# Optimization experiments

Measured on AMD Instinct MI355X. Metric: run time of the kernel, lower is better.

Reference implementation:

```python
import jax, jax.numpy as jnp
import numpy as np
import math

B, S, D = 1, 4096, 512
H, KVH, DH = 8, 4, 64
DH2 = DH // 2
M = int(math.isqrt(S))           # product-key grid side, S == M*M
K = 8                            # top_k
ROPE_BASE = 10000.0


def rope_cos_sin(seq_len, dh, base):
    inv_freq = 1.0 / (base ** (jnp.arange(0, dh, 2, dtype=jnp.float32) / dh))
    t = jnp.arange(seq_len, dtype=jnp.float32)
    freqs = jnp.outer(t, inv_freq)                      # (S, dh/2)
    emb = jnp.concatenate([freqs, freqs], axis=-1)      # (S, dh)
    return jnp.cos(emb), jnp.sin(emb)


def apply_rope(x, cos, sin):
    # x: (B, H, S, dh); half-split rotation (llama-style)
    dh2 = x.shape[-1] // 2
    rot = jnp.concatenate([-x[..., dh2:], x[..., :dh2]], axis=-1)
    return x * cos + rot * sin


def setup_inputs() -> dict:
    key = jax.random.key(0)
    ks = jax.random.split(key, 5)
    s = 0.02
    x = jax.random.normal(ks[0], (B, S, D), dtype=jnp.float32)
    Wq = jax.random.normal(ks[1], (H * DH, D), dtype=jnp.float32) * s
    Wk = jax.random.normal(ks[2], (KVH * DH, D), dtype=jnp.float32) * s
    Wv = jax.random.normal(ks[3], (KVH * DH, D), dtype=jnp.float32) * s
    Wo = jax.random.normal(ks[4], (D, H * DH), dtype=jnp.float32) * s
    return {"x": x, "Wq": Wq, "Wk": Wk, "Wv": Wv, "Wo": Wo}


def reference(x, Wq, Wk, Wv, Wo):
    b, s, d = x.shape
    cos, sin = rope_cos_sin(s, DH, ROPE_BASE)
    q = (x @ Wq.T).reshape(b, s, H, DH).transpose(0, 2, 1, 3)      # (B,H,S,DH)
    k = (x @ Wk.T).reshape(b, s, KVH, DH).transpose(0, 2, 1, 3)    # (B,KVH,S,DH)
    v = (x @ Wv.T).reshape(b, s, KVH, DH).transpose(0, 2, 1, 3)
    q = apply_rope(q, cos, sin)
    k = apply_rope(k, cos, sin)
    rep = H // KVH                                                 # GQA repeat_kv
    k = jnp.repeat(k, rep, axis=1)                                 # (B,H,S,DH)
    v = jnp.repeat(v, rep, axis=1)

    # factorized product keys: sum over grid rows / cols
    kg = k.reshape(b, H, M, M, DH)
    k1 = kg[..., :DH2].sum(axis=-2)                                # (B,H,M,DH2)
    k2 = kg[..., DH2:].sum(axis=-3)                                # (B,H,M,DH2)
    q1, q2 = q[..., :DH2], q[..., DH2:]

    def topk_sel(qh, kh):  # qh: (S,DH2), kh: (M,DH2)
        scores = qh @ kh.T                                         # (S,M)
        _, idx = jax.lax.top_k(scores, K)                          # (S,K)
        return kh[idx], idx                                        # (S,K,DH2), (S,K)

    sel2 = jax.vmap(jax.vmap(topk_sel))
    k1v, i1 = sel2(q1, k1)                                         # (B,H,S,K,DH2)
    k2v, i2 = sel2(q2, k2)

    # cross-product candidates: (B,H,S,K,K,DH) -> (B,H,S,K*K,DH)
    c1 = jnp.broadcast_to(k1v[:, :, :, :, None, :], (b, H, s, K, K, DH2))
    c2 = jnp.broadcast_to(k2v[:, :, :, None, :, :], (b, H, s, K, K, DH2))
    cand = jnp.concatenate([c1, c2], axis=-1).reshape(b, H, s, K * K, DH)

    scores_final = jnp.einsum('bhsd,bhscd->bhsc', q, cand)         # (B,H,S,K*K)
    _, sel = jax.lax.top_k(scores_final, K)                        # (B,H,S,K)
    final_k = jnp.take_along_axis(cand, sel[..., None], axis=3)    # (B,H,S,K,DH)

    row = jnp.take_along_axis(i1, sel // K, axis=3)
    col = jnp.take_along_axis(i2, sel % K, axis=3)
    v_idx = row * M + col                                          # (B,H,S,K)
    final_v = jax.vmap(jax.vmap(lambda vb, ib: vb[ib]))(v, v_idx)  # (B,H,S,K,DH)

    attn = jax.nn.softmax(
        jnp.einsum('bhsd,bhskd->bhsk', q, final_k) / math.sqrt(DH), axis=-1)
    o = jnp.einsum('bhsk,bhskd->bhsd', attn, final_v)              # (B,H,S,DH)
    o = o.transpose(0, 2, 1, 3).reshape(b, s, H * DH)
    return o @ Wo.T
```

## Files before the change

kernel.cpp:

```cpp
#include <hip/hip_runtime.h>
#include <math.h>


static constexpr size_t OFF_P1   = 0;
static constexpr size_t OFF_P2   = 4194304;
static constexpr size_t OFF_Q    = 8388608;
static constexpr size_t OFF_K    = 10485760;
static constexpr size_t OFF_V    = 11534336;
static constexpr size_t OFF_COS  = 12582912;
static constexpr size_t OFF_SIN  = 12713984;
static constexpr size_t OFF_K1   = 12845056;
static constexpr size_t OFF_K2   = 12853248;
static constexpr size_t OFF_O    = 12861440;
static constexpr size_t OFF_PACK = 14958592;

#define LDB 132

__device__ __forceinline__ float rdlane_f(float v, int lane) {
  return __int_as_float(__builtin_amdgcn_readlane(__float_as_int(v), lane));
}

__global__ __launch_bounds__(256) void freq_table_kernel(float* __restrict__ cosT,
    float* __restrict__ sinT) {
  int idx = blockIdx.x * 256 + threadIdx.x;
  int s = idx >> 5;
  int dp = idx & 31;
  double e = (double)dp * (1.0 / 32.0);
  float pf = (float)pow(10000.0, e);
  float invf = 1.0f / pf;
  float argf = __fmul_rn((float)s, invf);
  cosT[idx] = (float)cos((double)argf);
  sinT[idx] = (float)sin((double)argf);
}

__global__ __launch_bounds__(256) void gemm128_qkv(const float* __restrict__ A,
    const float* __restrict__ Wq, const float* __restrict__ Wk,
    const float* __restrict__ Wv, float* __restrict__ C1,
    float* __restrict__ C2) {
  __shared__ float As[16 * LDB];
  __shared__ float Bs[16 * LDB];
  const int tid = threadIdx.x;
  const int z = blockIdx.z;
  const int k0 = z ? 384 : 0;
  const int k1 = z ? 512 : 384;
  float* __restrict__ C = z ? C2 : C1;
  const int bm = blockIdx.y, bn = blockIdx.x;
  const int lrow = tid >> 1;
  const int lko = (tid & 1) << 3;
  const int ty = tid >> 4;
  const int tx = tid & 15;
  const float* Bbase = (bn < 4) ? (Wq + ((size_t)bn * 128) * 512)
                     : (bn < 6) ? (Wk + ((size_t)(bn - 4) * 128) * 512)
                                : (Wv + ((size_t)(bn - 6) * 128) * 512);
  const float* Ap = A + (size_t)(bm * 128 + lrow) * 512 + lko;
  const float* Bp = Bbase + (size_t)lrow * 512 + lko;
  float acc[8][8] = {{0.f}};
  float4 a0 = *(const float4*)(Ap + k0);
  float4 a1 = *(const float4*)(Ap + k0 + 4);
  float4 b0 = *(const float4*)(Bp + k0);
  float4 b1 = *(const float4*)(Bp + k0 + 4);
  for (int kt = k0; kt < k1; kt += 16) {
    __syncthreads();
    As[(lko + 0) * LDB + lrow] = a0.x;
    As[(lko + 1) * LDB + lrow] = a0.y;
    As[(lko + 2) * LDB + lrow] = a0.z;
    As[(lko + 3) * LDB + lrow] = a0.w;
    As[(lko + 4) * LDB + lrow] = a1.x;
    As[(lko + 5) * LDB + lrow] = a1.y;
    As[(lko + 6) * LDB + lrow] = a1.z;
    As[(lko + 7) * LDB + lrow] = a1.w;
    Bs[(lko + 0) * LDB + lrow] = b0.x;
    Bs[(lko + 1) * LDB + lrow] = b0.y;
    Bs[(lko + 2) * LDB + lrow] = b0.z;
    Bs[(lko + 3) * LDB + lrow] = b0.w;
    Bs[(lko + 4) * LDB + lrow] = b1.x;
    Bs[(lko + 5) * LDB + lrow] = b1.y;
    Bs[(lko + 6) * LDB + lrow] = b1.z;
    Bs[(lko + 7) * LDB + lrow] = b1.w;
    __syncthreads();
    if (kt + 16 < k1) {
      a0 = *(const float4*)(Ap + kt + 16);
      a1 = *(const float4*)(Ap + kt + 20);
      b0 = *(const float4*)(Bp + kt + 16);
      b1 = *(const float4*)(Bp + kt + 20);
    }
    #pragma unroll
    for (int k = 0; k < 16; ++k) {
      float4 al = *(const float4*)(&As[k * LDB + (ty << 2)]);
      float4 ah = *(const float4*)(&As[k * LDB + 64 + (ty << 2)]);
      float4 bl = *(const float4*)(&Bs[k * LDB + (tx << 2)]);
      float4 bh = *(const float4*)(&Bs[k * LDB + 64 + (tx << 2)]);
      float af[8] = {al.x, al.y, al.z, al.w, ah.x, ah.y, ah.z, ah.w};
      float bf[8] = {bl.x, bl.y, bl.z, bl.w, bh.x, bh.y, bh.z, bh.w};
      #pragma unroll
      for (int i2 = 0; i2 < 8; ++i2)
        #pragma unroll
        for (int j2 = 0; j2 < 8; ++j2)
          acc[i2][j2] = fmaf(af[i2], bf[j2], acc[i2][j2]);
    }
  }
  #pragma unroll
  for (int i2 = 0; i2 < 8; ++i2) {
    int row = bm * 128 + ((i2 < 4) ? (ty << 2) + i2 : 64 + (ty << 2) + i2 - 4);
    float* Cp = C + (size_t)row * 1024 + bn * 128;
    *(float4*)(Cp + (tx << 2))      = make_float4(acc[i2][0], acc[i2][1], acc[i2][2], acc[i2][3]);
    *(float4*)(Cp + 64 + (tx << 2)) = make_float4(acc[i2][4], acc[i2][5], acc[i2][6], acc[i2][7]);
  }
}

__global__ __launch_bounds__(256) void gemm128_panel(const float* __restrict__ A,
    const float* __restrict__ B, float* __restrict__ C1, float* __restrict__ C2,
    int N, int ksplit) {
  __shared__ float As[16 * LDB];
  __shared__ float Bs[16 * LDB];
  const int tid = threadIdx.x;
  const int z = blockIdx.z;
  const int k0 = z ? ksplit : 0;
  const int k1 = z ? 512 : ksplit;
  float* __restrict__ C = z ? C2 : C1;
  const int bm = blockIdx.y, bn = blockIdx.x;
  const int lrow = tid >> 1;
  const int lko = (tid & 1) << 3;
  const int ty = tid >> 4;
  const int tx = tid & 15;
  const float* Ap = A + (size_t)(bm * 128 + lrow) * 512 + lko;
  const float* Bp = B + (size_t)(bn * 128 + lrow) * 512 + lko;
  float acc[8][8] = {{0.f}};
  float4 a0 = *(const float4*)(Ap + k0);
  float4 a1 = *(const float4*)(Ap + k0 + 4);
  float4 b0 = *(const float4*)(Bp + k0);
  float4 b1 = *(const float4*)(Bp + k0 + 4);
  for (int kt = k0; kt < k1; kt += 16) {
    __syncthreads();
    As[(lko + 0) * LDB + lrow] = a0.x;
    As[(lko + 1) * LDB + lrow] = a0.y;
    As[(lko + 2) * LDB + lrow] = a0.z;
    As[(lko + 3) * LDB + lrow] = a0.w;
    As[(lko + 4) * LDB + lrow] = a1.x;
    As[(lko + 5) * LDB + lrow] = a1.y;
    As[(lko + 6) * LDB + lrow] = a1.z;
    As[(lko + 7) * LDB + lrow] = a1.w;
    Bs[(lko + 0) * LDB + lrow] = b0.x;
    Bs[(lko + 1) * LDB + lrow] = b0.y;
    Bs[(lko + 2) * LDB + lrow] = b0.z;
    Bs[(lko + 3) * LDB + lrow] = b0.w;
    Bs[(lko + 4) * LDB + lrow] = b1.x;
    Bs[(lko + 5) * LDB + lrow] = b1.y;
    Bs[(lko + 6) * LDB + lrow] = b1.z;
    Bs[(lko + 7) * LDB + lrow] = b1.w;
    __syncthreads();
    if (kt + 16 < k1) {
      a0 = *(const float4*)(Ap + kt + 16);
      a1 = *(const float4*)(Ap + kt + 20);
      b0 = *(const float4*)(Bp + kt + 16);
      b1 = *(const float4*)(Bp + kt + 20);
    }
    #pragma unroll
    for (int k = 0; k < 16; ++k) {
      float4 al = *(const float4*)(&As[k * LDB + (ty << 2)]);
      float4 ah = *(const float4*)(&As[k * LDB + 64 + (ty << 2)]);
      float4 bl = *(const float4*)(&Bs[k * LDB + (tx << 2)]);
      float4 bh = *(const float4*)(&Bs[k * LDB + 64 + (tx << 2)]);
      float af[8] = {al.x, al.y, al.z, al.w, ah.x, ah.y, ah.z, ah.w};
      float bf[8] = {bl.x, bl.y, bl.z, bl.w, bh.x, bh.y, bh.z, bh.w};
      #pragma unroll
      for (int i2 = 0; i2 < 8; ++i2)
        #pragma unroll
        for (int j2 = 0; j2 < 8; ++j2)
          acc[i2][j2] = fmaf(af[i2], bf[j2], acc[i2][j2]);
    }
  }
  #pragma unroll
  for (int i2 = 0; i2 < 8; ++i2) {
    int row = bm * 128 + ((i2 < 4) ? (ty << 2) + i2 : 64 + (ty << 2) + i2 - 4);
    float* Cp = C + (size_t)row * N + bn * 128;
    *(float4*)(Cp + (tx << 2))      = make_float4(acc[i2][0], acc[i2][1], acc[i2][2], acc[i2][3]);
    *(float4*)(Cp + 64 + (tx << 2)) = make_float4(acc[i2][4], acc[i2][5], acc[i2][6], acc[i2][7]);
  }
}

__global__ __launch_bounds__(256) void combine_kernel(const float* __restrict__ p1,
    const float* __restrict__ p2, float* __restrict__ out) {
  int i = blockIdx.x * 256 + threadIdx.x;
  out[i] = __fadd_rn(p1[i], p2[i]);
}

__global__ __launch_bounds__(256) void rope_reshape_kernel(const float* __restrict__ p1,
    const float* __restrict__ p2, const float* __restrict__ cosT,
    const float* __restrict__ sinT, float* __restrict__ qb,
    float* __restrict__ kb, float* __restrict__ vb) {
  int idx = blockIdx.x * 256 + threadIdx.x;
  int s = idx >> 10;
  int n = idx & 1023;
  float val = __fadd_rn(p1[idx], p2[idx]);
  int d = n & 63;
  if (n < 768) {
    int dp = d & 31;
    float cs = cosT[(s << 5) + dp];
    float sn = sinT[(s << 5) + dp];
    int npart = (n - d) + ((d < 32) ? d + 32 : d - 32);
    int pidx = (s << 10) + npart;
    float partner = __fadd_rn(p1[pidx], p2[pidx]);
    float rot = (d < 32) ? -partner : partner;
    float out = __fadd_rn(__fmul_rn(val, cs), __fmul_rn(rot, sn));
    if (n < 512) {
      int h = n >> 6;
      qb[((size_t)(h * 4096 + s) << 6) + d] = out;
    } else {
      int kvh = (n - 512) >> 6;
      kb[((size_t)(kvh * 4096 + s) << 6) + d] = out;
    }
  } else {
    int kvh = (n - 768) >> 6;
    vb[((size_t)(kvh * 4096 + s) << 6) + d] = val;
  }
}

__global__ __launch_bounds__(256) void k12_np_kernel(const float* __restrict__ kb,
    float* __restrict__ k1t, float* __restrict__ k2t) {
  int id = blockIdx.x * 256 + threadIdx.x;
  int which = id >> 13;
  int rem = id & 8191;
  int kvh = rem >> 11;
  int rem2 = rem & 2047;
  int i = rem2 >> 5;
  int d = rem2 & 31;
  const float* base = kb + ((size_t)(kvh * 4096) << 6);
  if (which == 0) {
    float acc = base[((size_t)(i * 64) << 6) + d];
    for (int c = 1; c < 64; ++c)
      acc = __fadd_rn(acc, base[((size_t)(i * 64 + c) << 6) + d]);
    k1t[(kvh * 64 + i) * 32 + d] = acc;
  } else {
    float acc = base[((size_t)i << 6) + d + 32];
    for (int r = 1; r < 64; ++r)
      acc = __fadd_rn(acc, base[((size_t)(r * 64 + i) << 6) + d + 32]);
    k2t[(kvh * 64 + i) * 32 + d] = acc;
  }
}

__global__ __launch_bounds__(256) void stage1_sel_kernel(
    const float* __restrict__ qb, const float* __restrict__ k1t,
    const float* __restrict__ k2t, unsigned long long* __restrict__ packs) {
  __shared__ float smem[8704];
  float* qs = smem;
  float* kd = smem + 4352;
  const int t = threadIdx.x;
  const int h = blockIdx.y;
  const int s0 = blockIdx.x * 64;
  const int kvh = h >> 1;
  #pragma unroll
  for (int i = 0; i < 16; ++i) {
    int j = t + i * 256;
    int ss = j >> 6, d = j & 63;
    qs[d * 68 + ss] = qb[((size_t)(h * 4096 + s0 + ss) << 6) + d];
  }
  #pragma unroll
  for (int i = 0; i < 8; ++i) {
    int j = t + i * 256;
    int r = j >> 5, d = j & 31;
    kd[d * 132 + r]      = k1t[(kvh * 64 + r) * 32 + d];
    kd[d * 132 + 64 + r] = k2t[(kvh * 64 + r) * 32 + d];
  }
  __syncthreads();
  const int ty = t >> 4;
  const int tx = t & 15;
  float acc1[4][4] = {{0.f}};
  float acc2[4][4] = {{0.f}};
  #pragma unroll
  for (int dp = 0; dp < 32; ++dp) {
    float4 kv1 = *(const float4*)&kd[dp * 132 + (ty << 2)];
    float4 kv2 = *(const float4*)&kd[dp * 132 + 64 + (ty << 2)];
    float4 q1 = *(const float4*)&qs[dp * 68 + (tx << 2)];
    float4 q2 = *(const float4*)&qs[(32 + dp) * 68 + (tx << 2)];
    float k1f[4] = {kv1.x, kv1.y, kv1.z, kv1.w};
    float k2f[4] = {kv2.x, kv2.y, kv2.z, kv2.w};
    float q1f[4] = {q1.x, q1.y, q1.z, q1.w};
    float q2f[4] = {q2.x, q2.y, q2.z, q2.w};
    #pragma unroll
    for (int i2 = 0; i2 < 4; ++i2)
      #pragma unroll
      for (int j2 = 0; j2 < 4; ++j2) {
        acc1[i2][j2] = fmaf(k1f[i2], q1f[j2], acc1[i2][j2]);
        acc2[i2][j2] = fmaf(k2f[i2], q2f[j2], acc2[i2][j2]);
      }
  }
  __syncthreads();
  float* sct = smem;
  #pragma unroll
  for (int i2 = 0; i2 < 4; ++i2) {
    int r = (ty << 2) + i2;
    *(float4*)&sct[(size_t)r * 68 + (tx << 2)] =
        make_float4(acc1[i2][0], acc1[i2][1], acc1[i2][2], acc1[i2][3]);
    *(float4*)&sct[(size_t)(64 + r) * 68 + (tx << 2)] =
        make_float4(acc2[i2][0], acc2[i2][1], acc2[i2][2], acc2[i2][3]);
  }
  __syncthreads();
  if (t < 128) {
    int set = t >> 6;
    int sq = t & 63;
    const float* p = sct + (size_t)(set << 6) * 68 + sq;
    float top[8];
    int idx[8];
    #pragma unroll
    for (int u = 0; u < 8; ++u) { top[u] = -INFINITY; idx[u] = 0; }
    #pragma unroll
    for (int r = 0; r < 64; ++r) {
      float v = p[(size_t)r * 68];
      int i = r;
      #pragma unroll
      for (int j = 0; j < 8; ++j) {
        bool gt = v > top[j];
        float tv = top[j]; int ti = idx[j];
        top[j] = gt ? v : tv;
        idx[j] = gt ? i : ti;
        v = gt ? tv : v;
        i = gt ? ti : i;
      }
    }
    unsigned long long pp = 0;
    #pragma unroll
    for (int u = 0; u < 8; ++u) pp |= (unsigned long long)idx[u] << (6 * u);
    packs[(((size_t)(h * 4096 + s0 + sq)) << 1) + set] = pp;
  }
}

__device__ __forceinline__ void bitonic64_val_desc(float& v, int lane) {
  #pragma unroll
  for (int k = 2; k <= 64; k <<= 1) {
    #pragma unroll
    for (int j = k >> 1; j >= 1; j >>= 1) {
      float ov = __shfl_xor(v, j, 64);
      bool up = ((lane & k) == 0) == ((lane & j) == 0);
      float mx = fmaxf(v, ov), mn = fminf(v, ov);
      v = up ? mx : mn;
    }
  }
}

__global__ __launch_bounds__(256) void attn_sel2_kernel(
    const ulonglong2* __restrict__ packs, const float* __restrict__ qb,
    const float* __restrict__ vb, const float* __restrict__ k1t,
    const float* __restrict__ k2t, float* __restrict__ ob) {
  const int lane = threadIdx.x & 63;
  const int w = blockIdx.x * 4 + (threadIdx.x >> 6);
  const int h = w >> 12;
  const int s = w & 4095;
  const int kvh = h >> 1;
  ulonglong2 pk = packs[w];
  const unsigned long long pack1 = pk.x, pack2 = pk.y;
  const float qv = qb[((size_t)w << 6) + lane];

  int r1 = (int)((pack1 >> (6 * (lane >> 3))) & 63);
  int r2 = (int)((pack2 >> (6 * (lane & 7))) & 63);
  const float* k1p = k1t + (size_t)(kvh * 64 + r1) * 32;
  const float* k2p = k2t + (size_t)(kvh * 64 + r2) * 32;
  float c = 0.f;
  #pragma unroll
  for (int dq = 0; dq < 32; dq += 4) {
    float4 kk = *(const float4*)(k1p + dq);
    c = __fadd_rn(c, __fmul_rn(rdlane_f(qv, dq + 0), kk.x));
    c = __fadd_rn(c, __fmul_rn(rdlane_f(qv, dq + 1), kk.y));
    c = __fadd_rn(c, __fmul_rn(rdlane_f(qv, dq + 2), kk.z));
    c = __fadd_rn(c, __fmul_rn(rdlane_f(qv, dq + 3), kk.w));
  }
  #pragma unroll
  for (int dq = 0; dq < 32; dq += 4) {
    float4 kk = *(const float4*)(k2p + dq);
    c = __fadd_rn(c, __fmul_rn(rdlane_f(qv, 32 + dq + 0), kk.x));
    c = __fadd_rn(c, __fmul_rn(rdlane_f(qv, 32 + dq + 1), kk.y));
    c = __fadd_rn(c, __fmul_rn(rdlane_f(qv, 32 + dq + 2), kk.z));
    c = __fadd_rn(c, __fmul_rn(rdlane_f(qv, 32 + dq + 3), kk.w));
  }
  const float scand = c;
  float v3 = c;
  bitonic64_val_desc(v3, lane);
  float cvs[8]; int ccs[8];
  unsigned long long used = 0;
  #pragma unroll
  for (int t = 0; t < 8; ++t) {
    float tv = rdlane_f(v3, t);
    unsigned long long m = __ballot(scand == tv) & ~used;
    int ix = __ffsll((long long)m) - 1;
    used |= 1ull << ix;
    cvs[t] = tv;
    ccs[t] = ix;
  }
  float y[8];
  #pragma unroll
  for (int t = 0; t < 8; ++t) y[t] = cvs[t] * 0.125f;
  float mx = y[0];
  #pragma unroll
  for (int t = 1; t < 8; ++t) if (y[t] > mx) mx = y[t];
  float e[8];
  #pragma unroll
  for (int t = 0; t < 8; ++t) e[t] = __expf(__fsub_rn(y[t], mx));
  float wsum = __fadd_rn(__fadd_rn(__fadd_rn(e[0], e[1]), __fadd_rn(e[2], e[3])),
                         __fadd_rn(__fadd_rn(e[4], e[5]), __fadd_rn(e[6], e[7])));
  const float* vbh = vb + ((size_t)kvh << 18);
  float o = 0.f;
  #pragma unroll
  for (int t = 0; t < 8; ++t) {
    float att = __fdiv_rn(e[t], wsum);
    int row = (int)((pack1 >> (6 * (ccs[t] >> 3))) & 63);
    int col = (int)((pack2 >> (6 * (ccs[t] & 7))) & 63);
    o = __fadd_rn(o, __fmul_rn(att, vbh[((size_t)(row * 64 + col) << 6) + lane]));
  }
  ob[(size_t)s * 512 + (h << 6) + lane] = o;
}

extern "C" void kernel_launch(void* const* d_in, const int* in_sizes, int n_in,
                              void* d_out, int out_size, void* d_ws, size_t ws_size,
                              hipStream_t stream) {
  const float* x  = (const float*)d_in[0];
  const float* Wq = (const float*)d_in[1];
  const float* Wk = (const float*)d_in[2];
  const float* Wv = (const float*)d_in[3];
  const float* Wo = (const float*)d_in[4];
  float* ws = (float*)d_ws;
  float* p1   = ws + OFF_P1;
  float* p2   = ws + OFF_P2;
  float* qb   = ws + OFF_Q;
  float* kb   = ws + OFF_K;
  float* vb   = ws + OFF_V;
  float* cosT = ws + OFF_COS;
  float* sinT = ws + OFF_SIN;
  float* k1t  = ws + OFF_K1;
  float* k2t  = ws + OFF_K2;
  float* ob   = ws + OFF_O;
  float* op1  = ws + OFF_P2;
  float* op2  = ws + OFF_P2 + 2097152;
  unsigned long long* packs = (unsigned long long*)(ws + OFF_PACK);

  freq_table_kernel<<<512, 256, 0, stream>>>(cosT, sinT);
  gemm128_qkv<<<dim3(8, 32, 2), 256, 0, stream>>>(x, Wq, Wk, Wv, p1, p2);
  rope_reshape_kernel<<<16384, 256, 0, stream>>>(p1, p2, cosT, sinT, qb, kb, vb);
  k12_np_kernel<<<64, 256, 0, stream>>>(kb, k1t, k2t);
  stage1_sel_kernel<<<dim3(64, 8), 256, 0, stream>>>(qb, k1t, k2t, packs);
  attn_sel2_kernel<<<8192, 256, 0, stream>>>((const ulonglong2*)packs, qb, vb, k1t, k2t, ob);
  gemm128_panel<<<dim3(4, 32, 2), 256, 0, stream>>>(ob, Wo, op1, op2, 512, 256);
  combine_kernel<<<8192, 256, 0, stream>>>(op1, op2, (float*)d_out);
}
```

Baseline: 241.6 us.

## Fuse Q RoPE into consumers, double-buffer GEMM LDS, split output GEMM four ways

The Q projection is no longer materialised as a roped buffer. Both the stage-1 selection kernel and the attention kernel now read the split-K partials, add them and apply RoPE on the fly, so the RoPE kernel only handles K and V. Both GEMMs use double-buffered shared memory, which removes one barrier per k-step. The output projection is split into four K chunks that reuse the old P1/P2 workspace, followed by a four-way combine. The cost is more redundant partial reads and RoPE arithmetic in the consumer kernels, twice the LDS per GEMM block, and more partial-sum traffic in the combine.

```diff
diff --git a/kernel.cpp b/kernel.cpp
--- a/kernel.cpp
+++ b/kernel.cpp
@@ -4,17 +4,17 @@
 
 static constexpr size_t OFF_P1   = 0;
 static constexpr size_t OFF_P2   = 4194304;
-static constexpr size_t OFF_Q    = 8388608;
-static constexpr size_t OFF_K    = 10485760;
-static constexpr size_t OFF_V    = 11534336;
-static constexpr size_t OFF_COS  = 12582912;
-static constexpr size_t OFF_SIN  = 12713984;
-static constexpr size_t OFF_K1   = 12845056;
-static constexpr size_t OFF_K2   = 12853248;
-static constexpr size_t OFF_O    = 12861440;
-static constexpr size_t OFF_PACK = 14958592;
+static constexpr size_t OFF_KB   = 8388608;
+static constexpr size_t OFF_V    = 9437184;
+static constexpr size_t OFF_COS  = 10485760;
+static constexpr size_t OFF_SIN  = 10616832;
+static constexpr size_t OFF_K1   = 10747904;
+static constexpr size_t OFF_K2   = 10756096;
+static constexpr size_t OFF_O    = 10764288;
+static constexpr size_t OFF_PACK = 12861440;
 
 #define LDB 132
+#define TILE_F (16 * LDB)
 
 __device__ __forceinline__ float rdlane_f(float v, int lane) {
   return __int_as_float(__builtin_amdgcn_readlane(__float_as_int(v), lane));
@@ -37,8 +37,8 @@
     const float* __restrict__ Wq, const float* __restrict__ Wk,
     const float* __restrict__ Wv, float* __restrict__ C1,
     float* __restrict__ C2) {
-  __shared__ float As[16 * LDB];
-  __shared__ float Bs[16 * LDB];
+  __shared__ float As[2 * TILE_F];
+  __shared__ float Bs[2 * TILE_F];
   const int tid = threadIdx.x;
   const int z = blockIdx.z;
   const int k0 = z ? 384 : 0;
@@ -59,24 +59,26 @@
   float4 a1 = *(const float4*)(Ap + k0 + 4);
   float4 b0 = *(const float4*)(Bp + k0);
   float4 b1 = *(const float4*)(Bp + k0 + 4);
+  int p = 0;
   for (int kt = k0; kt < k1; kt += 16) {
-    __syncthreads();
-    As[(lko + 0) * LDB + lrow] = a0.x;
-    As[(lko + 1) * LDB + lrow] = a0.y;
-    As[(lko + 2) * LDB + lrow] = a0.z;
-    As[(lko + 3) * LDB + lrow] = a0.w;
-    As[(lko + 4) * LDB + lrow] = a1.x;
-    As[(lko + 5) * LDB + lrow] = a1.y;
-    As[(lko + 6) * LDB + lrow] = a1.z;
-    As[(lko + 7) * LDB + lrow] = a1.w;
-    Bs[(lko + 0) * LDB + lrow] = b0.x;
-    Bs[(lko + 1) * LDB + lrow] = b0.y;
-    Bs[(lko + 2) * LDB + lrow] = b0.z;
-    Bs[(lko + 3) * LDB + lrow] = b0.w;
-    Bs[(lko + 4) * LDB + lrow] = b1.x;
-    Bs[(lko + 5) * LDB + lrow] = b1.y;
-    Bs[(lko + 6) * LDB + lrow] = b1.z;
-    Bs[(lko + 7) * LDB + lrow] = b1.w;
+    float* Asp = As + p * TILE_F;
+    float* Bsp = Bs + p * TILE_F;
+    Asp[(lko + 0) * LDB + lrow] = a0.x;
+    Asp[(lko + 1) * LDB + lrow] = a0.y;
+    Asp[(lko + 2) * LDB + lrow] = a0.z;
+    Asp[(lko + 3) * LDB + lrow] = a0.w;
+    Asp[(lko + 4) * LDB + lrow] = a1.x;
+    Asp[(lko + 5) * LDB + lrow] = a1.y;
+    Asp[(lko + 6) * LDB + lrow] = a1.z;
+    Asp[(lko + 7) * LDB + lrow] = a1.w;
+    Bsp[(lko + 0) * LDB + lrow] = b0.x;
+    Bsp[(lko + 1) * LDB + lrow] = b0.y;
+    Bsp[(lko + 2) * LDB + lrow] = b0.z;
+    Bsp[(lko + 3) * LDB + lrow] = b0.w;
+    Bsp[(lko + 4) * LDB + lrow] = b1.x;
+    Bsp[(lko + 5) * LDB + lrow] = b1.y;
+    Bsp[(lko + 6) * LDB + lrow] = b1.z;
+    Bsp[(lko + 7) * LDB + lrow] = b1.w;
     __syncthreads();
     if (kt + 16 < k1) {
       a0 = *(const float4*)(Ap + kt + 16);
@@ -86,10 +88,10 @@
     }
     #pragma unroll
     for (int k = 0; k < 16; ++k) {
-      float4 al = *(const float4*)(&As[k * LDB + (ty << 2)]);
-      float4 ah = *(const float4*)(&As[k * LDB + 64 + (ty << 2)]);
-      float4 bl = *(const float4*)(&Bs[k * LDB + (tx << 2)]);
-      float4 bh = *(const float4*)(&Bs[k * LDB + 64 + (tx << 2)]);
+      float4 al = *(const float4*)(&Asp[k * LDB + (ty << 2)]);
+      float4 ah = *(const float4*)(&Asp[k * LDB + 64 + (ty << 2)]);
+      float4 bl = *(const float4*)(&Bsp[k * LDB + (tx << 2)]);
+      float4 bh = *(const float4*)(&Bsp[k * LDB + 64 + (tx << 2)]);
       float af[8] = {al.x, al.y, al.z, al.w, ah.x, ah.y, ah.z, ah.w};
       float bf[8] = {bl.x, bl.y, bl.z, bl.w, bh.x, bh.y, bh.z, bh.w};
       #pragma unroll
@@ -98,6 +100,7 @@
         for (int j2 = 0; j2 < 8; ++j2)
           acc[i2][j2] = fmaf(af[i2], bf[j2], acc[i2][j2]);
     }
+    p ^= 1;
   }
   #pragma unroll
   for (int i2 = 0; i2 < 8; ++i2) {
@@ -108,16 +111,15 @@
   }
 }
 
-__global__ __launch_bounds__(256) void gemm128_panel(const float* __restrict__ A,
-    const float* __restrict__ B, float* __restrict__ C1, float* __restrict__ C2,
-    int N, int ksplit) {
-  __shared__ float As[16 * LDB];
-  __shared__ float Bs[16 * LDB];
+__global__ __launch_bounds__(256) void gemm128_out(const float* __restrict__ A,
+    const float* __restrict__ B, float* __restrict__ Cbase, int N) {
+  __shared__ float As[2 * TILE_F];
+  __shared__ float Bs[2 * TILE_F];
   const int tid = threadIdx.x;
   const int z = blockIdx.z;
-  const int k0 = z ? ksplit : 0;
-  const int k1 = z ? 512 : ksplit;
-  float* __restrict__ C = z ? C2 : C1;
+  const int k0 = z << 7;
+  const int k1 = k0 + 128;
+  float* __restrict__ C = Cbase + (size_t)z * ((size_t)4096 * N);
   const int bm = blockIdx.y, bn = blockIdx.x;
   const int lrow = tid >> 1;
   const int lko = (tid & 1) << 3;
@@ -130,24 +132,26 @@
   float4 a1 = *(const float4*)(Ap + k0 + 4);
   float4 b0 = *(const float4*)(Bp + k0);
   float4 b1 = *(const float4*)(Bp + k0 + 4);
+  int p = 0;
   for (int kt = k0; kt < k1; kt += 16) {
-    __syncthreads();
-    As[(lko + 0) * LDB + lrow] = a0.x;
-    As[(lko + 1) * LDB + lrow] = a0.y;
-    As[(lko + 2) * LDB + lrow] = a0.z;
-    As[(lko + 3) * LDB + lrow] = a0.w;
-    As[(lko + 4) * LDB + lrow] = a1.x;
-    As[(lko + 5) * LDB + lrow] = a1.y;
-    As[(lko + 6) * LDB + lrow] = a1.z;
-    As[(lko + 7) * LDB + lrow] = a1.w;
-    Bs[(lko + 0) * LDB + lrow] = b0.x;
-    Bs[(lko + 1) * LDB + lrow] = b0.y;
-    Bs[(lko + 2) * LDB + lrow] = b0.z;
-    Bs[(lko + 3) * LDB + lrow] = b0.w;
-    Bs[(lko + 4) * LDB + lrow] = b1.x;
-    Bs[(lko + 5) * LDB + lrow] = b1.y;
-    Bs[(lko + 6) * LDB + lrow] = b1.z;
-    Bs[(lko + 7) * LDB + lrow] = b1.w;
+    float* Asp = As + p * TILE_F;
+    float* Bsp = Bs + p * TILE_F;
+    Asp[(lko + 0) * LDB + lrow] = a0.x;
+    Asp[(lko + 1) * LDB + lrow] = a0.y;
+    Asp[(lko + 2) * LDB + lrow] = a0.z;
+    Asp[(lko + 3) * LDB + lrow] = a0.w;
+    Asp[(lko + 4) * LDB + lrow] = a1.x;
+    Asp[(lko + 5) * LDB + lrow] = a1.y;
+    Asp[(lko + 6) * LDB + lrow] = a1.z;
+    Asp[(lko + 7) * LDB + lrow] = a1.w;
+    Bsp[(lko + 0) * LDB + lrow] = b0.x;
+    Bsp[(lko + 1) * LDB + lrow] = b0.y;
+    Bsp[(lko + 2) * LDB + lrow] = b0.z;
+    Bsp[(lko + 3) * LDB + lrow] = b0.w;
+    Bsp[(lko + 4) * LDB + lrow] = b1.x;
+    Bsp[(lko + 5) * LDB + lrow] = b1.y;
+    Bsp[(lko + 6) * LDB + lrow] = b1.z;
+    Bsp[(lko + 7) * LDB + lrow] = b1.w;
     __syncthreads();
     if (kt + 16 < k1) {
       a0 = *(const float4*)(Ap + kt + 16);
@@ -157,10 +161,10 @@
     }
     #pragma unroll
     for (int k = 0; k < 16; ++k) {
-      float4 al = *(const float4*)(&As[k * LDB + (ty << 2)]);
-      float4 ah = *(const float4*)(&As[k * LDB + 64 + (ty << 2)]);
-      float4 bl = *(const float4*)(&Bs[k * LDB + (tx << 2)]);
-      float4 bh = *(const float4*)(&Bs[k * LDB + 64 + (tx << 2)]);
+      float4 al = *(const float4*)(&Asp[k * LDB + (ty << 2)]);
+      float4 ah = *(const float4*)(&Asp[k * LDB + 64 + (ty << 2)]);
+      float4 bl = *(const float4*)(&Bsp[k * LDB + (tx << 2)]);
+      float4 bh = *(const float4*)(&Bsp[k * LDB + 64 + (tx << 2)]);
       float af[8] = {al.x, al.y, al.z, al.w, ah.x, ah.y, ah.z, ah.w};
       float bf[8] = {bl.x, bl.y, bl.z, bl.w, bh.x, bh.y, bh.z, bh.w};
       #pragma unroll
@@ -169,6 +173,7 @@
         for (int j2 = 0; j2 < 8; ++j2)
           acc[i2][j2] = fmaf(af[i2], bf[j2], acc[i2][j2]);
     }
+    p ^= 1;
   }
   #pragma unroll
   for (int i2 = 0; i2 < 8; ++i2) {
@@ -179,37 +184,32 @@
   }
 }
 
-__global__ __launch_bounds__(256) void combine_kernel(const float* __restrict__ p1,
-    const float* __restrict__ p2, float* __restrict__ out) {
+__global__ __launch_bounds__(256) void combine4_kernel(const float* __restrict__ o0,
+    const float* __restrict__ o1, const float* __restrict__ o2,
+    const float* __restrict__ o3, float* __restrict__ out) {
   int i = blockIdx.x * 256 + threadIdx.x;
-  out[i] = __fadd_rn(p1[i], p2[i]);
-}
-
-__global__ __launch_bounds__(256) void rope_reshape_kernel(const float* __restrict__ p1,
+  out[i] = __fadd_rn(__fadd_rn(__fadd_rn(o0[i], o1[i]), o2[i]), o3[i]);
+}
+
+__global__ __launch_bounds__(256) void kv_rope_kernel(const float* __restrict__ p1,
     const float* __restrict__ p2, const float* __restrict__ cosT,
-    const float* __restrict__ sinT, float* __restrict__ qb,
-    float* __restrict__ kb, float* __restrict__ vb) {
-  int idx = blockIdx.x * 256 + threadIdx.x;
-  int s = idx >> 10;
-  int n = idx & 1023;
+    const float* __restrict__ sinT, float* __restrict__ kb,
+    float* __restrict__ vb) {
+  int id = blockIdx.x * 256 + threadIdx.x;
+  int s = id >> 9;
+  int n = 512 + (id & 511);
+  int idx = (s << 10) + n;
   float val = __fadd_rn(p1[idx], p2[idx]);
   int d = n & 63;
   if (n < 768) {
-    int dp = d & 31;
-    float cs = cosT[(s << 5) + dp];
-    float sn = sinT[(s << 5) + dp];
-    int npart = (n - d) + ((d < 32) ? d + 32 : d - 32);
-    int pidx = (s << 10) + npart;
-    float partner = __fadd_rn(p1[pidx], p2[pidx]);
-    float rot = (d < 32) ? -partner : partner;
+    int pidx = idx ^ 32;
+    float pv = __fadd_rn(p1[pidx], p2[pidx]);
+    float cs = cosT[(s << 5) + (d & 31)];
+    float sn = sinT[(s << 5) + (d & 31)];
+    float rot = (d < 32) ? -pv : pv;
     float out = __fadd_rn(__fmul_rn(val, cs), __fmul_rn(rot, sn));
-    if (n < 512) {
-      int h = n >> 6;
-      qb[((size_t)(h * 4096 + s) << 6) + d] = out;
-    } else {
-      int kvh = (n - 512) >> 6;
-      kb[((size_t)(kvh * 4096 + s) << 6) + d] = out;
-    }
+    int kvh = (n - 512) >> 6;
+    kb[((size_t)(kvh * 4096 + s) << 6) + d] = out;
   } else {
     int kvh = (n - 768) >> 6;
     vb[((size_t)(kvh * 4096 + s) << 6) + d] = val;
@@ -240,8 +240,10 @@
 }
 
 __global__ __launch_bounds__(256) void stage1_sel_kernel(
-    const float* __restrict__ qb, const float* __restrict__ k1t,
-    const float* __restrict__ k2t, unsigned long long* __restrict__ packs) {
+    const float* __restrict__ p1, const float* __restrict__ p2,
+    const float* __restrict__ cosT, const float* __restrict__ sinT,
+    const float* __restrict__ k1t, const float* __restrict__ k2t,
+    unsigned long long* __restrict__ packs) {
   __shared__ float smem[8704];
   float* qs = smem;
   float* kd = smem + 4352;
@@ -253,7 +255,14 @@
   for (int i = 0; i < 16; ++i) {
     int j = t + i * 256;
     int ss = j >> 6, d = j & 63;
-    qs[d * 68 + ss] = qb[((size_t)(h * 4096 + s0 + ss) << 6) + d];
+    int s = s0 + ss;
+    int idx = (s << 10) + (h << 6) + d;
+    float val = __fadd_rn(p1[idx], p2[idx]);
+    float pv  = __fadd_rn(p1[idx ^ 32], p2[idx ^ 32]);
+    float cs = cosT[(s << 5) + (d & 31)];
+    float sn = sinT[(s << 5) + (d & 31)];
+    float rot = (d < 32) ? -pv : pv;
+    qs[d * 68 + ss] = __fadd_rn(__fmul_rn(val, cs), __fmul_rn(rot, sn));
   }
   #pragma unroll
   for (int i = 0; i < 8; ++i) {
@@ -339,9 +348,11 @@
 }
 
 __global__ __launch_bounds__(256) void attn_sel2_kernel(
-    const ulonglong2* __restrict__ packs, const float* __restrict__ qb,
-    const float* __restrict__ vb, const float* __restrict__ k1t,
-    const float* __restrict__ k2t, float* __restrict__ ob) {
+    const ulonglong2* __restrict__ packs, const float* __restrict__ p1,
+    const float* __restrict__ p2, const float* __restrict__ cosT,
+    const float* __restrict__ sinT, const float* __restrict__ vb,
+    const float* __restrict__ k1t, const float* __restrict__ k2t,
+    float* __restrict__ ob) {
   const int lane = threadIdx.x & 63;
   const int w = blockIdx.x * 4 + (threadIdx.x >> 6);
   const int h = w >> 12;
@@ -349,7 +360,13 @@
   const int kvh = h >> 1;
   ulonglong2 pk = packs[w];
   const unsigned long long pack1 = pk.x, pack2 = pk.y;
-  const float qv = qb[((size_t)w << 6) + lane];
+  int qidx = (s << 10) + (h << 6) + lane;
+  float vraw = __fadd_rn(p1[qidx], p2[qidx]);
+  float pv = __shfl_xor(vraw, 32, 64);
+  float cs = cosT[(s << 5) + (lane & 31)];
+  float sn = sinT[(s << 5) + (lane & 31)];
+  float rot = (lane < 32) ? -pv : pv;
+  const float qv = __fadd_rn(__fmul_rn(vraw, cs), __fmul_rn(rot, sn));
 
   int r1 = (int)((pack1 >> (6 * (lane >> 3))) & 63);
   int r2 = (int)((pack2 >> (6 * (lane & 7))) & 63);
@@ -420,24 +437,24 @@
   float* ws = (float*)d_ws;
   float* p1   = ws + OFF_P1;
   float* p2   = ws + OFF_P2;
-  float* qb   = ws + OFF_Q;
-  float* kb   = ws + OFF_K;
+  float* kb   = ws + OFF_KB;
   float* vb   = ws + OFF_V;
   float* cosT = ws + OFF_COS;
   float* sinT = ws + OFF_SIN;
   float* k1t  = ws + OFF_K1;
   float* k2t  = ws + OFF_K2;
   float* ob   = ws + OFF_O;
-  float* op1  = ws + OFF_P2;
-  float* op2  = ws + OFF_P2 + 2097152;
   unsigned long long* packs = (unsigned long long*)(ws + OFF_PACK);
+  float* op = ws + OFF_P1;
 
   freq_table_kernel<<<512, 256, 0, stream>>>(cosT, sinT);
   gemm128_qkv<<<dim3(8, 32, 2), 256, 0, stream>>>(x, Wq, Wk, Wv, p1, p2);
-  rope_reshape_kernel<<<16384, 256, 0, stream>>>(p1, p2, cosT, sinT, qb, kb, vb);
+  kv_rope_kernel<<<8192, 256, 0, stream>>>(p1, p2, cosT, sinT, kb, vb);
   k12_np_kernel<<<64, 256, 0, stream>>>(kb, k1t, k2t);
-  stage1_sel_kernel<<<dim3(64, 8), 256, 0, stream>>>(qb, k1t, k2t, packs);
-  attn_sel2_kernel<<<8192, 256, 0, stream>>>((const ulonglong2*)packs, qb, vb, k1t, k2t, ob);
-  gemm128_panel<<<dim3(4, 32, 2), 256, 0, stream>>>(ob, Wo, op1, op2, 512, 256);
-  combine_kernel<<<8192, 256, 0, stream>>>(op1, op2, (float*)d_out);
-}
+  stage1_sel_kernel<<<dim3(64, 8), 256, 0, stream>>>(p1, p2, cosT, sinT, k1t, k2t, packs);
+  attn_sel2_kernel<<<8192, 256, 0, stream>>>((const ulonglong2*)packs, p1, p2,
+                                             cosT, sinT, vb, k1t, k2t, ob);
+  gemm128_out<<<dim3(4, 32, 4), 256, 0, stream>>>(ob, Wo, op, 512);
+  combine4_kernel<<<8192, 256, 0, stream>>>(op, op + 2097152, op + 4194304,
+                                            op + 6291456, (float*)d_out);
+}
```

Result: no change. 237.2 us (median of 2 runs) (-1.8%).

## Fuse split-K combine and RoPE into consumers, drop rope_reshape pass

Applied to the files above, without the earlier changes.

Removes the standalone rope_reshape kernel and the q/k/v intermediate buffers. Each consumer (k1/k2 reduction, stage1 selection, attention) now sums the two split-K QKV partials and applies RoPE on the fly. The output projection is also split four ways along K instead of two, with a four-way combine. This avoids a full read/write pass over the QKV tensor, at the cost of redundant partial-sum reads, strided access in the k12 reduction, and more partial-output traffic in the output GEMM.

```diff
diff --git a/kernel.cpp b/kernel.cpp
--- a/kernel.cpp
+++ b/kernel.cpp
@@ -4,15 +4,12 @@
 
 static constexpr size_t OFF_P1   = 0;
 static constexpr size_t OFF_P2   = 4194304;
-static constexpr size_t OFF_Q    = 8388608;
-static constexpr size_t OFF_K    = 10485760;
-static constexpr size_t OFF_V    = 11534336;
-static constexpr size_t OFF_COS  = 12582912;
-static constexpr size_t OFF_SIN  = 12713984;
-static constexpr size_t OFF_K1   = 12845056;
-static constexpr size_t OFF_K2   = 12853248;
-static constexpr size_t OFF_O    = 12861440;
-static constexpr size_t OFF_PACK = 14958592;
+static constexpr size_t OFF_COS  = 8388608;
+static constexpr size_t OFF_SIN  = 8519680;
+static constexpr size_t OFF_K1   = 8650752;
+static constexpr size_t OFF_K2   = 8658944;
+static constexpr size_t OFF_O    = 8667136;
+static constexpr size_t OFF_PACK = 10764288;
 
 #define LDB 132
 
@@ -108,16 +105,15 @@
   }
 }
 
-__global__ __launch_bounds__(256) void gemm128_panel(const float* __restrict__ A,
-    const float* __restrict__ B, float* __restrict__ C1, float* __restrict__ C2,
-    int N, int ksplit) {
+__global__ __launch_bounds__(256) void gemm128_out(const float* __restrict__ A,
+    const float* __restrict__ B, float* __restrict__ Cbase, int N) {
   __shared__ float As[16 * LDB];
   __shared__ float Bs[16 * LDB];
   const int tid = threadIdx.x;
   const int z = blockIdx.z;
-  const int k0 = z ? ksplit : 0;
-  const int k1 = z ? 512 : ksplit;
-  float* __restrict__ C = z ? C2 : C1;
+  const int k0 = z << 7;
+  const int k1 = k0 + 128;
+  float* __restrict__ C = Cbase + (size_t)z * ((size_t)4096 * N);
   const int bm = blockIdx.y, bn = blockIdx.x;
   const int lrow = tid >> 1;
   const int lko = (tid & 1) << 3;
@@ -179,45 +175,17 @@
   }
 }
 
-__global__ __launch_bounds__(256) void combine_kernel(const float* __restrict__ p1,
-    const float* __restrict__ p2, float* __restrict__ out) {
+__global__ __launch_bounds__(256) void combine4_kernel(const float* __restrict__ o0,
+    const float* __restrict__ o1, const float* __restrict__ o2,
+    const float* __restrict__ o3, float* __restrict__ out) {
   int i = blockIdx.x * 256 + threadIdx.x;
-  out[i] = __fadd_rn(p1[i], p2[i]);
-}
-
-__global__ __launch_bounds__(256) void rope_reshape_kernel(const float* __restrict__ p1,
+  out[i] = __fadd_rn(__fadd_rn(__fadd_rn(o0[i], o1[i]), o2[i]), o3[i]);
+}
+
+__global__ __launch_bounds__(256) void k12_rope_kernel(const float* __restrict__ p1,
     const float* __restrict__ p2, const float* __restrict__ cosT,
-    const float* __restrict__ sinT, float* __restrict__ qb,
-    float* __restrict__ kb, float* __restrict__ vb) {
-  int idx = blockIdx.x * 256 + threadIdx.x;
-  int s = idx >> 10;
-  int n = idx & 1023;
-  float val = __fadd_rn(p1[idx], p2[idx]);
-  int d = n & 63;
-  if (n < 768) {
-    int dp = d & 31;
-    float cs = cosT[(s << 5) + dp];
-    float sn = sinT[(s << 5) + dp];
-    int npart = (n - d) + ((d < 32) ? d + 32 : d - 32);
-    int pidx = (s << 10) + npart;
-    float partner = __fadd_rn(p1[pidx], p2[pidx]);
-    float rot = (d < 32) ? -partner : partner;
-    float out = __fadd_rn(__fmul_rn(val, cs), __fmul_rn(rot, sn));
-    if (n < 512) {
-      int h = n >> 6;
-      qb[((size_t)(h * 4096 + s) << 6) + d] = out;
-    } else {
-      int kvh = (n - 512) >> 6;
-      kb[((size_t)(kvh * 4096 + s) << 6) + d] = out;
-    }
-  } else {
-    int kvh = (n - 768) >> 6;
-    vb[((size_t)(kvh * 4096 + s) << 6) + d] = val;
-  }
-}
-
-__global__ __launch_bounds__(256) void k12_np_kernel(const float* __restrict__ kb,
-    float* __restrict__ k1t, float* __restrict__ k2t) {
+    const float* __restrict__ sinT, float* __restrict__ k1t,
+    float* __restrict__ k2t) {
   int id = blockIdx.x * 256 + threadIdx.x;
   int which = id >> 13;
   int rem = id & 8191;
@@ -225,23 +193,41 @@
   int rem2 = rem & 2047;
   int i = rem2 >> 5;
   int d = rem2 & 31;
-  const float* base = kb + ((size_t)(kvh * 4096) << 6);
+  float acc = 0.f;
   if (which == 0) {
-    float acc = base[((size_t)(i * 64) << 6) + d];
-    for (int c = 1; c < 64; ++c)
-      acc = __fadd_rn(acc, base[((size_t)(i * 64 + c) << 6) + d]);
+    #pragma unroll 4
+    for (int c = 0; c < 64; ++c) {
+      int s = i * 64 + c;
+      int idx = (s << 10) + 512 + (kvh << 6) + d;
+      float val = __fadd_rn(p1[idx], p2[idx]);
+      float pv  = __fadd_rn(p1[idx ^ 32], p2[idx ^ 32]);
+      float cs = cosT[(s << 5) + d];
+      float sn = sinT[(s << 5) + d];
+      float e = __fadd_rn(__fmul_rn(val, cs), __fmul_rn(-pv, sn));
+      acc = (c == 0) ? e : __fadd_rn(acc, e);
+    }
     k1t[(kvh * 64 + i) * 32 + d] = acc;
   } else {
-    float acc = base[((size_t)i << 6) + d + 32];
-    for (int r = 1; r < 64; ++r)
-      acc = __fadd_rn(acc, base[((size_t)(r * 64 + i) << 6) + d + 32]);
+    #pragma unroll 4
+    for (int r = 0; r < 64; ++r) {
+      int s = r * 64 + i;
+      int idx = (s << 10) + 512 + (kvh << 6) + d + 32;
+      float val = __fadd_rn(p1[idx], p2[idx]);
+      float pv  = __fadd_rn(p1[idx ^ 32], p2[idx ^ 32]);
+      float cs = cosT[(s << 5) + d];
+      float sn = sinT[(s << 5) + d];
+      float e = __fadd_rn(__fmul_rn(val, cs), __fmul_rn(pv, sn));
+      acc = (r == 0) ? e : __fadd_rn(acc, e);
+    }
     k2t[(kvh * 64 + i) * 32 + d] = acc;
   }
 }
 
 __global__ __launch_bounds__(256) void stage1_sel_kernel(
-    const float* __restrict__ qb, const float* __restrict__ k1t,
-    const float* __restrict__ k2t, unsigned long long* __restrict__ packs) {
+    const float* __restrict__ p1, const float* __restrict__ p2,
+    const float* __restrict__ cosT, const float* __restrict__ sinT,
+    const float* __restrict__ k1t, const float* __restrict__ k2t,
+    unsigned long long* __restrict__ packs) {
   __shared__ float smem[8704];
   float* qs = smem;
   float* kd = smem + 4352;
@@ -253,7 +239,14 @@
   for (int i = 0; i < 16; ++i) {
     int j = t + i * 256;
     int ss = j >> 6, d = j & 63;
-    qs[d * 68 + ss] = qb[((size_t)(h * 4096 + s0 + ss) << 6) + d];
+    int s = s0 + ss;
+    int idx = (s << 10) + (h << 6) + d;
+    float val = __fadd_rn(p1[idx], p2[idx]);
+    float pv  = __fadd_rn(p1[idx ^ 32], p2[idx ^ 32]);
+    float cs = cosT[(s << 5) + (d & 31)];
+    float sn = sinT[(s << 5) + (d & 31)];
+    float rot = (d < 32) ? -pv : pv;
+    qs[d * 68 + ss] = __fadd_rn(__fmul_rn(val, cs), __fmul_rn(rot, sn));
   }
   #pragma unroll
   for (int i = 0; i < 8; ++i) {
@@ -339,8 +332,9 @@
 }
 
 __global__ __launch_bounds__(256) void attn_sel2_kernel(
-    const ulonglong2* __restrict__ packs, const float* __restrict__ qb,
-    const float* __restrict__ vb, const float* __restrict__ k1t,
+    const ulonglong2* __restrict__ packs, const float* __restrict__ p1,
+    const float* __restrict__ p2, const float* __restrict__ cosT,
+    const float* __restrict__ sinT, const float* __restrict__ k1t,
     const float* __restrict__ k2t, float* __restrict__ ob) {
   const int lane = threadIdx.x & 63;
   const int w = blockIdx.x * 4 + (threadIdx.x >> 6);
@@ -349,7 +343,13 @@
   const int kvh = h >> 1;
   ulonglong2 pk = packs[w];
   const unsigned long long pack1 = pk.x, pack2 = pk.y;
-  const float qv = qb[((size_t)w << 6) + lane];
+  int qidx = (s << 10) + (h << 6) + lane;
+  float vraw = __fadd_rn(p1[qidx], p2[qidx]);
+  float pv = __shfl_xor(vraw, 32, 64);
+  float cs = cosT[(s << 5) + (lane & 31)];
+  float sn = sinT[(s << 5) + (lane & 31)];
+  float rot = (lane < 32) ? -pv : pv;
+  const float qv = __fadd_rn(__fmul_rn(vraw, cs), __fmul_rn(rot, sn));
 
   int r1 = (int)((pack1 >> (6 * (lane >> 3))) & 63);
   int r2 = (int)((pack2 >> (6 * (lane & 7))) & 63);
@@ -397,14 +397,16 @@
   for (int t = 0; t < 8; ++t) e[t] = __expf(__fsub_rn(y[t], mx));
   float wsum = __fadd_rn(__fadd_rn(__fadd_rn(e[0], e[1]), __fadd_rn(e[2], e[3])),
                          __fadd_rn(__fadd_rn(e[4], e[5]), __fadd_rn(e[6], e[7])));
-  const float* vbh = vb + ((size_t)kvh << 18);
   float o = 0.f;
   #pragma unroll
   for (int t = 0; t < 8; ++t) {
     float att = __fdiv_rn(e[t], wsum);
     int row = (int)((pack1 >> (6 * (ccs[t] >> 3))) & 63);
     int col = (int)((pack2 >> (6 * (ccs[t] & 7))) & 63);
-    o = __fadd_rn(o, __fmul_rn(att, vbh[((size_t)(row * 64 + col) << 6) + lane]));
+    int sv = row * 64 + col;
+    int vidx = (sv << 10) + 768 + (kvh << 6) + lane;
+    float vv = __fadd_rn(p1[vidx], p2[vidx]);
+    o = __fadd_rn(o, __fmul_rn(att, vv));
   }
   ob[(size_t)s * 512 + (h << 6) + lane] = o;
 }
@@ -420,24 +422,21 @@
   float* ws = (float*)d_ws;
   float* p1   = ws + OFF_P1;
   float* p2   = ws + OFF_P2;
-  float* qb   = ws + OFF_Q;
-  float* kb   = ws + OFF_K;
-  float* vb   = ws + OFF_V;
   float* cosT = ws + OFF_COS;
   float* sinT = ws + OFF_SIN;
   float* k1t  = ws + OFF_K1;
   float* k2t  = ws + OFF_K2;
   float* ob   = ws + OFF_O;
-  float* op1  = ws + OFF_P2;
-  float* op2  = ws + OFF_P2 + 2097152;
   unsigned long long* packs = (unsigned long long*)(ws + OFF_PACK);
+  float* op = ws + OFF_P1;
 
   freq_table_kernel<<<512, 256, 0, stream>>>(cosT, sinT);
   gemm128_qkv<<<dim3(8, 32, 2), 256, 0, stream>>>(x, Wq, Wk, Wv, p1, p2);
-  rope_reshape_kernel<<<16384, 256, 0, stream>>>(p1, p2, cosT, sinT, qb, kb, vb);
-  k12_np_kernel<<<64, 256, 0, stream>>>(kb, k1t, k2t);
-  stage1_sel_kernel<<<dim3(64, 8), 256, 0, stream>>>(qb, k1t, k2t, packs);
-  attn_sel2_kernel<<<8192, 256, 0, stream>>>((const ulonglong2*)packs, qb, vb, k1t, k2t, ob);
-  gemm128_panel<<<dim3(4, 32, 2), 256, 0, stream>>>(ob, Wo, op1, op2, 512, 256);
-  combine_kernel<<<8192, 256, 0, stream>>>(op1, op2, (float*)d_out);
-}
+  k12_rope_kernel<<<64, 256, 0, stream>>>(p1, p2, cosT, sinT, k1t, k2t);
+  stage1_sel_kernel<<<dim3(64, 8), 256, 0, stream>>>(p1, p2, cosT, sinT, k1t, k2t, packs);
+  attn_sel2_kernel<<<8192, 256, 0, stream>>>((const ulonglong2*)packs, p1, p2,
+                                             cosT, sinT, k1t, k2t, ob);
+  gemm128_out<<<dim3(4, 32, 4), 256, 0, stream>>>(ob, Wo, op, 512);
+  combine4_kernel<<<8192, 256, 0, stream>>>(op, op + 2097152, op + 4194304,
+                                            op + 6291456, (float*)d_out);
+}
```

Measured after the change: 241.2 us. Within noise of the previous version (-0.2%).
